# Kernel optimization log

Hardware: AMD Instinct MI355X
Metric: run time of the kernel (lower is better)

Reference implementation:

```python
import jax, jax.numpy as jnp
import numpy as np

N = 50000
E = 800000
N_IN = 256
N_HID = 128
N_OUT = 64
HOP = 10


def setup_inputs() -> dict:
    key = jax.random.key(0)
    ks = jax.random.split(key, 12)
    x = jax.random.normal(ks[0], (N, N_IN), dtype=jnp.float32)
    s = jax.random.randint(ks[1], (E,), 0, N, dtype=jnp.int32)
    t = jax.random.randint(ks[2], (E,), 0, N, dtype=jnp.int32)
    # parameters (xavier-ish scaling)
    fc1W = jax.random.normal(ks[3], (N_HID, N_IN), dtype=jnp.float32) * (1.0 / np.sqrt(N_IN))
    fc1b = jnp.zeros((N_HID,), dtype=jnp.float32)
    fcsW = jax.random.normal(ks[4], (HOP, N_HID, N_HID), dtype=jnp.float32) * (1.0 / np.sqrt(N_HID))
    fcsb = jnp.zeros((HOP, N_HID), dtype=jnp.float32)
    a1 = jax.random.normal(ks[5], (HOP, N_HID), dtype=jnp.float32) * (1.0 / np.sqrt(N_HID))
    a2 = jax.random.normal(ks[6], (HOP, N_HID), dtype=jnp.float32) * (1.0 / np.sqrt(N_HID))
    fc2W = jax.random.normal(ks[7], (N_OUT, N_HID), dtype=jnp.float32) * (1.0 / np.sqrt(N_HID))
    fc2b = jnp.zeros((N_OUT,), dtype=jnp.float32)
    return {"x": x, "s": s, "t": t, "fc1W": fc1W, "fc1b": fc1b,
            "fcsW": fcsW, "fcsb": fcsb, "a1": a1, "a2": a2,
            "fc2W": fc2W, "fc2b": fc2b}


def reference(x, s, t, fc1W, fc1b, fcsW, fcsb, a1, a2, fc2W, fc2b):
    # dropout layers are identity in eval mode
    x = jax.nn.relu(x @ fc1W.T + fc1b)  # [N, n_hid]
    h = x
    for i in range(HOP):
        W, b = fcsW[i], fcsb[i]
        x_new = x @ W.T + b          # [N, n_hid]
        h = h @ W.T + b              # [N, n_hid]
        x1 = x_new @ a1[i]           # [N]
        h1 = h @ a2[i]               # [N]
        w1 = jnp.exp(jax.nn.leaky_relu(x1[s] + h1[t], 0.2))       # [E]
        w2 = jnp.exp(jax.nn.leaky_relu(x1 + x_new @ a2[i], 0.2))  # [N]
        div = jax.ops.segment_sum(w1, s, num_segments=N) + w2     # [N]
        num = jax.ops.segment_sum(w1[:, None] * h[t], s, num_segments=N) + w2[:, None] * x_new
        h = jax.nn.elu(num / div[:, None])
    return h @ fc2W.T + fc2b  # [N, n_out]
```

## Files before the change

### kernel.cpp

```cpp
#include <hip/hip_runtime.h>
#include <math.h>


typedef __attribute__((ext_vector_type(8))) short short8;
typedef __attribute__((ext_vector_type(4))) float f32x4;
#define MFMA16 __builtin_amdgcn_mfma_f32_16x16x32_bf16

__device__ __forceinline__ float lrelu02(float v) { return v > 0.f ? v : 0.2f * v; }

__device__ __forceinline__ float2 bf2f2(unsigned int v) {
    return make_float2(__uint_as_float(v << 16), __uint_as_float(v & 0xffff0000u));
}
__device__ __forceinline__ unsigned int f2bf(float f) {
    unsigned int u = __float_as_uint(f);
    u += 0x7fffu + ((u >> 16) & 1u);
    return u >> 16;
}
__device__ __forceinline__ float hi_part(float f) {
    return __uint_as_float(__float_as_uint(f) & 0xffff0000u);
}
__device__ __forceinline__ uint4 pack_hi(const float4& a, const float4& b) {
    uint4 r;
    r.x = (__float_as_uint(a.x) >> 16) | (__float_as_uint(a.y) & 0xffff0000u);
    r.y = (__float_as_uint(a.z) >> 16) | (__float_as_uint(a.w) & 0xffff0000u);
    r.z = (__float_as_uint(b.x) >> 16) | (__float_as_uint(b.y) & 0xffff0000u);
    r.w = (__float_as_uint(b.z) >> 16) | (__float_as_uint(b.w) & 0xffff0000u);
    return r;
}
__device__ __forceinline__ uint4 pack_lo(const float4& a, const float4& b) {
    uint4 r;
    r.x = f2bf(a.x - hi_part(a.x)) | (f2bf(a.y - hi_part(a.y)) << 16);
    r.y = f2bf(a.z - hi_part(a.z)) | (f2bf(a.w - hi_part(a.w)) << 16);
    r.z = f2bf(b.x - hi_part(b.x)) | (f2bf(b.y - hi_part(b.y)) << 16);
    r.w = f2bf(b.z - hi_part(b.z)) | (f2bf(b.w - hi_part(b.w)) << 16);
    return r;
}

__global__ __launch_bounds__(256) void k_count(const int* __restrict__ s, int* __restrict__ cnt, int E) {
    int e = blockIdx.x * 256 + threadIdx.x;
    if (e < E) atomicAdd(&cnt[s[e]], 1);
}

__global__ __launch_bounds__(256) void k_scan1(const int* __restrict__ cnt, int* __restrict__ bs, int N) {
    __shared__ int sh[256];
    int idx = blockIdx.x * 256 + threadIdx.x;
    sh[threadIdx.x] = (idx < N) ? cnt[idx] : 0;
    __syncthreads();
#pragma unroll
    for (int off = 128; off; off >>= 1) {
        if (threadIdx.x < off) sh[threadIdx.x] += sh[threadIdx.x + off];
        __syncthreads();
    }
    if (threadIdx.x == 0) bs[blockIdx.x] = sh[0];
}

__global__ __launch_bounds__(256) void k_scan2(int* __restrict__ bs, int G) {
    __shared__ int sh[256];
    int t = threadIdx.x;
    int v = (t < G) ? bs[t] : 0;
    sh[t] = v;
    __syncthreads();
    int val = v;
#pragma unroll
    for (int off = 1; off < 256; off <<= 1) {
        int o = (t >= off) ? sh[t - off] : 0;
        __syncthreads();
        val += o; sh[t] = val;
        __syncthreads();
    }
    if (t < G) bs[t] = val - v;
}

__global__ __launch_bounds__(256) void k_scan3(const int* __restrict__ cnt, const int* __restrict__ bs,
                                               int* __restrict__ rp, int N) {
    __shared__ int sh[256];
    int t = threadIdx.x;
    int idx = blockIdx.x * 256 + t;
    int v = (idx < N) ? cnt[idx] : 0;
    sh[t] = v;
    __syncthreads();
    int val = v;
#pragma unroll
    for (int off = 1; off < 256; off <<= 1) {
        int o = (t >= off) ? sh[t - off] : 0;
        __syncthreads();
        val += o; sh[t] = val;
        __syncthreads();
    }
    if (idx <= N) rp[idx] = val - v + bs[blockIdx.x];
}

__global__ __launch_bounds__(256) void k_scatter(const int* __restrict__ s, const int* __restrict__ t,
                                                 const int* __restrict__ rp, int* __restrict__ cursor,
                                                 int* __restrict__ t_sorted, int E) {
    int e = blockIdx.x * 256 + threadIdx.x;
    if (e < E) {
        int u = s[e];
        int pos = atomicAdd(&cursor[u], 1);
        t_sorted[rp[u] + pos] = t[e];
    }
}

__global__ __launch_bounds__(256) void k_wsplit(const float* __restrict__ W,
                                                unsigned short* __restrict__ Whi,
                                                unsigned short* __restrict__ Wlo, int total) {
    int i = blockIdx.x * 256 + threadIdx.x;
    if (i < total) {
        float f = W[i];
        unsigned int u = __float_as_uint(f);
        Whi[i] = (unsigned short)(u >> 16);
        Wlo[i] = (unsigned short)f2bf(f - __uint_as_float(u & 0xffff0000u));
    }
}

__global__ __launch_bounds__(256) void k_prep(
    const float* __restrict__ fcsW, const float* __restrict__ fcsb,
    const float* __restrict__ a1, const float* __restrict__ a2,
    float* __restrict__ Vf, unsigned short* __restrict__ Vh,
    unsigned short* __restrict__ Vl, float* __restrict__ cvec) {
    int i = blockIdx.x;
    int t = threadIdx.x;
    const float* W = fcsW + (size_t)i * 16384;
    if (t < 128) {
        float s1 = 0.f, s2 = 0.f;
        for (int j = 0; j < 128; ++j) {
            float w = W[j * 128 + t];
            s1 = fmaf(w, a1[i * 128 + j], s1);
            s2 = fmaf(w, a2[i * 128 + j], s2);
        }
        Vf[i * 128 + t] = s1;
        Vf[(16 + i) * 128 + t] = s2;
        Vh[i * 128 + t] = (unsigned short)(__float_as_uint(s1) >> 16);
        Vl[i * 128 + t] = (unsigned short)f2bf(s1 - hi_part(s1));
        Vh[(16 + i) * 128 + t] = (unsigned short)(__float_as_uint(s2) >> 16);
        Vl[(16 + i) * 128 + t] = (unsigned short)f2bf(s2 - hi_part(s2));
    } else if (t == 128) {
        float c1 = 0.f, c2 = 0.f;
        for (int j = 0; j < 128; ++j) {
            c1 = fmaf(fcsb[i * 128 + j], a1[i * 128 + j], c1);
            c2 = fmaf(fcsb[i * 128 + j], a2[i * 128 + j], c2);
        }
        cvec[i] = c1;
        cvec[16 + i] = c2;
    }
}

__global__ __launch_bounds__(256) void k_fc1(
    const float* __restrict__ Xf,
    const unsigned short* __restrict__ Wh, const unsigned short* __restrict__ Wl,
    const float* __restrict__ bias,
    unsigned short* __restrict__ Yhi, unsigned short* __restrict__ Ylo, int N) {
    const int tid = threadIdx.x;
    const int r0 = blockIdx.x * 64;
    const int lane = tid & 63;
    const int w = tid >> 6;
    const int wr = (w >> 1) * 32, wc = (w & 1) * 64;
    const int frow = lane & 15;
    const int fk = lane >> 4;
    const int q4 = lane >> 4;

    f32x4 acc[2][4];
#pragma unroll
    for (int i = 0; i < 2; ++i)
#pragma unroll
        for (int j = 0; j < 4; ++j) acc[i][j] = (f32x4){0.f, 0.f, 0.f, 0.f};

    const float4 z4 = make_float4(0.f, 0.f, 0.f, 0.f);
#pragma unroll
    for (int kc = 0; kc < 8; ++kc) {
        short8 ah[2], al[2];
#pragma unroll
        for (int ri = 0; ri < 2; ++ri) {
            int row = r0 + wr + ri * 16 + frow;
            float4 va = z4, vb = z4;
            if (row < N) {
                const float* p = Xf + (size_t)row * 256 + kc * 32 + fk * 8;
                va = *(const float4*)p;
                vb = *(const float4*)(p + 4);
            }
            uint4 h = pack_hi(va, vb);
            uint4 l = pack_lo(va, vb);
            ah[ri] = *(short8*)&h;
            al[ri] = *(short8*)&l;
        }
#pragma unroll
        for (int ci = 0; ci < 4; ++ci) {
            int col = wc + ci * 16 + frow;
            short8 bh = *(const short8*)(Wh + (size_t)col * 256 + kc * 32 + fk * 8);
            short8 bl = *(const short8*)(Wl + (size_t)col * 256 + kc * 32 + fk * 8);
#pragma unroll
            for (int ri = 0; ri < 2; ++ri) {
                acc[ri][ci] = MFMA16(ah[ri], bh, acc[ri][ci], 0, 0, 0);
                acc[ri][ci] = MFMA16(ah[ri], bl, acc[ri][ci], 0, 0, 0);
                acc[ri][ci] = MFMA16(al[ri], bh, acc[ri][ci], 0, 0, 0);
            }
        }
    }

#pragma unroll
    for (int ci = 0; ci < 4; ++ci) {
        int col = wc + ci * 16 + frow;
        float bcol = bias[col];
#pragma unroll
        for (int ri = 0; ri < 2; ++ri) {
            f32x4 v = acc[ri][ci];
#pragma unroll
            for (int reg = 0; reg < 4; ++reg) {
                int grow = r0 + wr + ri * 16 + q4 * 4 + reg;
                if (grow < N) {
                    float val = fmaxf(v[reg] + bcol, 0.f);
                    Yhi[(size_t)grow * 128 + col] = (unsigned short)(__float_as_uint(val) >> 16);
                    Ylo[(size_t)grow * 128 + col] = (unsigned short)f2bf(val - hi_part(val));
                }
            }
        }
    }
}

__global__ __launch_bounds__(256) void k_xdots(
    const unsigned short* __restrict__ Xhi, const unsigned short* __restrict__ Xlo,
    const unsigned short* __restrict__ Vh, const unsigned short* __restrict__ Vl,
    const float* __restrict__ cvec,
    float* __restrict__ x1a_all, float* __restrict__ xa2a_all, int N) {
    const int tid = threadIdx.x;
    const int r0 = blockIdx.x * 64;
    const int lane = tid & 63;
    const int w = tid >> 6;
    const int wr = w * 16;
    const int frow = lane & 15;
    const int fk = lane >> 4;
    const int q4 = lane >> 4;

    f32x4 acc[2];
    acc[0] = (f32x4){0.f, 0.f, 0.f, 0.f};
    acc[1] = (f32x4){0.f, 0.f, 0.f, 0.f};

    const short8 z8 = (short8){0, 0, 0, 0, 0, 0, 0, 0};
#pragma unroll
    for (int kc = 0; kc < 4; ++kc) {
        int row = r0 + wr + frow;
        bool ok = row < N;
        short8 ah = ok ? *(const short8*)(Xhi + (size_t)row * 128 + kc * 32 + fk * 8) : z8;
        short8 al = ok ? *(const short8*)(Xlo + (size_t)row * 128 + kc * 32 + fk * 8) : z8;
#pragma unroll
        for (int ci = 0; ci < 2; ++ci) {
            int col = ci * 16 + frow;
            short8 bh = *(const short8*)(Vh + (size_t)col * 128 + kc * 32 + fk * 8);
            short8 bl = *(const short8*)(Vl + (size_t)col * 128 + kc * 32 + fk * 8);
            acc[ci] = MFMA16(ah, bh, acc[ci], 0, 0, 0);
            acc[ci] = MFMA16(ah, bl, acc[ci], 0, 0, 0);
            acc[ci] = MFMA16(al, bh, acc[ci], 0, 0, 0);
        }
    }

#pragma unroll
    for (int ci = 0; ci < 2; ++ci) {
        int col = ci * 16 + frow;
        float c = cvec[col];
#pragma unroll
        for (int reg = 0; reg < 4; ++reg) {
            int grow = r0 + wr + q4 * 4 + reg;
            if (grow < N) {
                float val = acc[ci][reg] + c;
                if (col < 10) x1a_all[(size_t)col * N + grow] = val;
                else if (col >= 16 && col < 26) xa2a_all[(size_t)(col - 16) * N + grow] = val;
            }
        }
    }
}

__global__ __launch_bounds__(256) void k_gemm(
    const unsigned short* __restrict__ G,
    const unsigned short* __restrict__ Wh, const unsigned short* __restrict__ Wl,
    const float* __restrict__ bias, const float* __restrict__ vnext,
    const float* __restrict__ cnextp,
    unsigned short* __restrict__ Hout, float* __restrict__ h1a, int N) {
    __shared__ unsigned short So[64 * 128];
    __shared__ float dotbuf[64][2];
    const int tid = threadIdx.x;
    const int r0 = blockIdx.x * 64;
    const int lane = tid & 63;
    const int w = tid >> 6;
    const int wr = (w >> 1) * 32, wc = (w & 1) * 64;
    const int frow = lane & 15;
    const int fk = lane >> 4;
    const int q4 = lane >> 4;
    const bool dodot = vnext != nullptr;

    f32x4 acc[2][4];
#pragma unroll
    for (int i = 0; i < 2; ++i)
#pragma unroll
        for (int j = 0; j < 4; ++j) acc[i][j] = (f32x4){0.f, 0.f, 0.f, 0.f};

    const short8 z8 = (short8){0, 0, 0, 0, 0, 0, 0, 0};
#pragma unroll
    for (int kc = 0; kc < 4; ++kc) {
        short8 ah[2];
#pragma unroll
        for (int ri = 0; ri < 2; ++ri) {
            int row = r0 + wr + ri * 16 + frow;
            ah[ri] = (row < N) ? *(const short8*)(G + (size_t)row * 128 + kc * 32 + fk * 8) : z8;
        }
#pragma unroll
        for (int ci = 0; ci < 4; ++ci) {
            int col = wc + ci * 16 + frow;
            short8 bh = *(const short8*)(Wh + (size_t)col * 128 + kc * 32 + fk * 8);
            short8 bl = *(const short8*)(Wl + (size_t)col * 128 + kc * 32 + fk * 8);
#pragma unroll
            for (int ri = 0; ri < 2; ++ri) {
                acc[ri][ci] = MFMA16(ah[ri], bh, acc[ri][ci], 0, 0, 0);
                acc[ri][ci] = MFMA16(ah[ri], bl, acc[ri][ci], 0, 0, 0);
            }
        }
    }

    float dotA[2][4] = {};
#pragma unroll
    for (int ci = 0; ci < 4; ++ci) {
        int col = wc + ci * 16 + frow;
        float bcol = bias[col];
        float vc = dodot ? vnext[col] : 0.f;
#pragma unroll
        for (int ri = 0; ri < 2; ++ri) {
            f32x4 v = acc[ri][ci];
#pragma unroll
            for (int reg = 0; reg < 4; ++reg) {
                float val = v[reg] + bcol;
                val = val > 0.f ? val : expf(val) - 1.f;
                int row = wr + ri * 16 + q4 * 4 + reg;
                int dw = (col >> 1) ^ ((row & 12) << 1);
                So[row * 128 + dw * 2 + (col & 1)] = (unsigned short)f2bf(val);
                dotA[ri][reg] = fmaf(val, vc, dotA[ri][reg]);
            }
        }
    }
#pragma unroll
    for (int m = 1; m < 16; m <<= 1)
#pragma unroll
        for (int ri = 0; ri < 2; ++ri)
#pragma unroll
            for (int reg = 0; reg < 4; ++reg)
                dotA[ri][reg] += __shfl_xor(dotA[ri][reg], m, 64);
    if (frow == 0) {
#pragma unroll
        for (int ri = 0; ri < 2; ++ri)
#pragma unroll
            for (int reg = 0; reg < 4; ++reg) {
                int rl = wr + ri * 16 + q4 * 4 + reg;
                dotbuf[rl][w & 1] = dotA[ri][reg];
            }
    }
    __syncthreads();

#pragma unroll
    for (int q = 0; q < 4; ++q) {
        int idx = q * 256 + tid;
        int row = idx >> 4;
        int gc = idx & 15;
        int dwb = (gc * 4) ^ ((row & 12) << 1);
        uint4 vv = *(const uint4*)(So + row * 128 + dwb * 2);
        int grow = r0 + row;
        if (grow < N) *(uint4*)(Hout + (size_t)grow * 128 + gc * 8) = vv;
    }
    if (dodot && tid < 64) {
        int grow = r0 + tid;
        if (grow < N) h1a[grow] = dotbuf[tid][0] + dotbuf[tid][1] + cnextp[0];
    }
}

__global__ __launch_bounds__(256) void k_agg(
    const unsigned short* __restrict__ xh, const unsigned short* __restrict__ xl,
    const unsigned short* __restrict__ table,
    const float* __restrict__ x1a, const float* __restrict__ xa2a,
    const float* __restrict__ h1a, const int* __restrict__ rp,
    const int* __restrict__ ts,
    unsigned short* __restrict__ g_out, int N) {
    __shared__ uint2 ew[4][64];
    const int wid = threadIdx.x >> 6;
    const int lane = threadIdx.x & 63;
    const int u = blockIdx.x * 4 + wid;
    if (u >= N) return;
    const int l2 = lane << 1;
    float x1u = x1a[u];
    float w2 = expf(lrelu02(x1u + xa2a[u]));
    unsigned int sh = *(const unsigned int*)(xh + (size_t)u * 128 + l2);
    unsigned int sl = *(const unsigned int*)(xl + (size_t)u * 128 + l2);
    float2 hx = bf2f2(sh), lx = bf2f2(sl);
    float accx = w2 * (hx.x + lx.x), accy = w2 * (hx.y + lx.y);
    float div = w2;
    int p0 = rp[u], p1 = rp[u + 1];
    for (int base = p0; base < p1; base += 64) {
        int e = base + lane;
        uint2 pk = make_uint2(0u, 0u);
        if (e < p1) {
            int tv = ts[e];
            pk.x = (unsigned int)tv;
            pk.y = __float_as_uint(expf(lrelu02(x1u + h1a[tv])));
        }
        ew[wid][lane] = pk;
        int m = p1 - base; if (m > 64) m = 64;
        int m8 = (m + 7) & ~7;
        for (int j = 0; j < m8; j += 8) {
            uint2 q[8];
#pragma unroll
            for (int k = 0; k < 8; ++k) q[k] = ew[wid][j + k];
            unsigned int hv[8];
#pragma unroll
            for (int k = 0; k < 8; ++k)
                hv[k] = *(const unsigned int*)(table + (size_t)q[k].x * 128 + l2);
#pragma unroll
            for (int k = 0; k < 8; ++k) {
                float ww = __uint_as_float(q[k].y);
                float2 f = bf2f2(hv[k]);
                accx = fmaf(ww, f.x, accx);
                accy = fmaf(ww, f.y, accy);
                div += ww;
            }
        }
    }
    float ox = accx / div, oy = accy / div;
    *(unsigned int*)(g_out + (size_t)u * 128 + l2) = f2bf(ox) | (f2bf(oy) << 16);
}

__global__ __launch_bounds__(256) void k_fc2(
    const unsigned short* __restrict__ Xhi,
    const unsigned short* __restrict__ Wh, const unsigned short* __restrict__ Wl,
    const float* __restrict__ bias, float* __restrict__ Yf, int N) {
    const int tid = threadIdx.x;
    const int r0 = blockIdx.x * 64;
    const int lane = tid & 63;
    const int w = tid >> 6;
    const int wr = w * 16;
    const int frow = lane & 15;
    const int fk = lane >> 4;
    const int q4 = lane >> 4;

    f32x4 acc[4];
#pragma unroll
    for (int j = 0; j < 4; ++j) acc[j] = (f32x4){0.f, 0.f, 0.f, 0.f};

    const short8 z8 = (short8){0, 0, 0, 0, 0, 0, 0, 0};
#pragma unroll
    for (int kc = 0; kc < 4; ++kc) {
        int row = r0 + wr + frow;
        short8 ah = (row < N) ? *(const short8*)(Xhi + (size_t)row * 128 + kc * 32 + fk * 8) : z8;
#pragma unroll
        for (int ci = 0; ci < 4; ++ci) {
            int col = ci * 16 + frow;
            short8 bh = *(const short8*)(Wh + (size_t)col * 128 + kc * 32 + fk * 8);
            short8 bl = *(const short8*)(Wl + (size_t)col * 128 + kc * 32 + fk * 8);
            acc[ci] = MFMA16(ah, bh, acc[ci], 0, 0, 0);
            acc[ci] = MFMA16(ah, bl, acc[ci], 0, 0, 0);
        }
    }

#pragma unroll
    for (int ci = 0; ci < 4; ++ci) {
        int col = ci * 16 + frow;
        float bcol = bias[col];
#pragma unroll
        for (int reg = 0; reg < 4; ++reg) {
            int grow = r0 + wr + q4 * 4 + reg;
            if (grow < N) Yf[(size_t)grow * 64 + col] = acc[ci][reg] + bcol;
        }
    }
}

extern "C" void kernel_launch(void* const* d_in, const int* in_sizes, int n_in,
                              void* d_out, int out_size, void* d_ws, size_t ws_size,
                              hipStream_t stream) {
    const float* x_in = (const float*)d_in[0];
    const int*   s    = (const int*)d_in[1];
    const int*   t    = (const int*)d_in[2];
    const float* fc1W = (const float*)d_in[3];
    const float* fc1b = (const float*)d_in[4];
    const float* fcsW = (const float*)d_in[5];
    const float* fcsb = (const float*)d_in[6];
    const float* a1   = (const float*)d_in[7];
    const float* a2   = (const float*)d_in[8];
    const float* fc2W = (const float*)d_in[9];
    const float* fc2b = (const float*)d_in[10];

    const int N = in_sizes[0] / 256;
    const int E = in_sizes[1];
    const int G = (N + 255) / 256;
    const int NB64 = (N + 63) / 64;

    char* ws = (char*)d_ws;
    size_t off = 0;
    auto alloc = [&](size_t bytes) -> void* {
        void* p = ws + off;
        off += (bytes + 255) & ~(size_t)255;
        return p;
    };
    unsigned short* xbuf_hi = (unsigned short*)alloc((size_t)N * 128 * 2);
    unsigned short* xbuf_lo = (unsigned short*)alloc((size_t)N * 128 * 2);
    unsigned short* h_hi    = (unsigned short*)alloc((size_t)N * 128 * 2);
    unsigned short* gbuf    = (unsigned short*)alloc((size_t)N * 128 * 2);
    unsigned short* Whi  = (unsigned short*)alloc((size_t)10 * 16384 * 2);
    unsigned short* Wlo  = (unsigned short*)alloc((size_t)10 * 16384 * 2);
    unsigned short* W1hi = (unsigned short*)alloc((size_t)128 * 256 * 2);
    unsigned short* W1lo = (unsigned short*)alloc((size_t)128 * 256 * 2);
    unsigned short* W2hi = (unsigned short*)alloc((size_t)64 * 128 * 2);
    unsigned short* W2lo = (unsigned short*)alloc((size_t)64 * 128 * 2);
    float* Vf   = (float*)alloc((size_t)32 * 128 * 4);
    unsigned short* Vh = (unsigned short*)alloc((size_t)32 * 128 * 2);
    unsigned short* Vl = (unsigned short*)alloc((size_t)32 * 128 * 2);
    float* cvec = (float*)alloc((size_t)32 * 4);
    float* x1a_all  = (float*)alloc((size_t)10 * N * 4);
    float* xa2a_all = (float*)alloc((size_t)10 * N * 4);
    float* h1a  = (float*)alloc((size_t)N * 4);
    int* row_ptr  = (int*)alloc((size_t)(N + 1) * 4);
    int* cnt      = (int*)alloc((size_t)N * 4);
    int* bsums    = (int*)alloc((size_t)1024);
    int* t_sorted = (int*)alloc((size_t)E * 4);

    hipMemsetAsync(cnt, 0, (size_t)N * 4, stream);
    k_count<<<(E + 255) / 256, 256, 0, stream>>>(s, cnt, E);
    k_scan1<<<G, 256, 0, stream>>>(cnt, bsums, N);
    k_scan2<<<1, 256, 0, stream>>>(bsums, G);
    k_scan3<<<G, 256, 0, stream>>>(cnt, bsums, row_ptr, N);
    hipMemsetAsync(cnt, 0, (size_t)N * 4, stream);
    k_scatter<<<(E + 255) / 256, 256, 0, stream>>>(s, t, row_ptr, cnt, t_sorted, E);

    k_wsplit<<<(10 * 16384 + 255) / 256, 256, 0, stream>>>(fcsW, Whi, Wlo, 10 * 16384);
    k_wsplit<<<(128 * 256 + 255) / 256, 256, 0, stream>>>(fc1W, W1hi, W1lo, 128 * 256);
    k_wsplit<<<(64 * 128 + 255) / 256, 256, 0, stream>>>(fc2W, W2hi, W2lo, 64 * 128);
    hipMemsetAsync(Vf, 0, (size_t)32 * 128 * 4, stream);
    hipMemsetAsync(Vh, 0, (size_t)32 * 128 * 2, stream);
    hipMemsetAsync(Vl, 0, (size_t)32 * 128 * 2, stream);
    hipMemsetAsync(cvec, 0, (size_t)32 * 4, stream);
    k_prep<<<10, 256, 0, stream>>>(fcsW, fcsb, a1, a2, Vf, Vh, Vl, cvec);

    k_fc1<<<NB64, 256, 0, stream>>>(x_in, W1hi, W1lo, fc1b, xbuf_hi, xbuf_lo, N);

    k_xdots<<<NB64, 256, 0, stream>>>(xbuf_hi, xbuf_lo, Vh, Vl, cvec,
                                      x1a_all, xa2a_all, N);

    for (int i = 0; i < 10; ++i) {
        const unsigned short* table = (i == 0) ? xbuf_hi : h_hi;
        const float* h1_i = (i == 0) ? (xa2a_all + 0) : h1a;
        k_agg<<<(N + 3) / 4, 256, 0, stream>>>(xbuf_hi, xbuf_lo, table,
                                               x1a_all + (size_t)i * N,
                                               xa2a_all + (size_t)i * N,
                                               h1_i, row_ptr, t_sorted, gbuf, N);
        const float* vnext = (i < 9) ? (Vf + (size_t)(16 + i + 1) * 128) : nullptr;
        const float* cnextp = cvec + (16 + i + 1);
        k_gemm<<<NB64, 256, 0, stream>>>(gbuf, Whi + (size_t)i * 16384,
                                         Wlo + (size_t)i * 16384,
                                         fcsb + (size_t)i * 128, vnext, cnextp,
                                         h_hi, h1a, N);
    }

    k_fc2<<<NB64, 256, 0, stream>>>(h_hi, W2hi, W2lo, fc2b, (float*)d_out, N);
}
```

Baseline: 806.3 us.

## Fuse edge aggregation into per-hop GEMM kernel with ping-pong h buffers

Merges the per-node softmax aggregation kernel and the following 128x128 GEMM into one k_hop kernel. Each 64-row block first aggregates neighbour features into shared memory, then runs MFMA directly from LDS. This removes the gbuf global round-trip and one launch per hop. Because h is now read by other blocks while being written, it ping-pongs between two h buffers and two h1 buffers. The fc1 epilogue is also changed to stage its output through swizzled LDS so it can store 16-byte vectors. Trade-offs: the 64-row grid has far fewer blocks than the old 4-rows-per-block aggregation, so load balance across irregular degrees may suffer. The self term also drops the lo-part of x, which slightly lowers precision.

```diff
diff --git a/kernel.cpp b/kernel.cpp
--- a/kernel.cpp
+++ b/kernel.cpp
@@ -150,6 +150,8 @@
     const unsigned short* __restrict__ Wh, const unsigned short* __restrict__ Wl,
     const float* __restrict__ bias,
     unsigned short* __restrict__ Yhi, unsigned short* __restrict__ Ylo, int N) {
+    __shared__ unsigned short Shi[64 * 128];
+    __shared__ unsigned short Slo[64 * 128];
     const int tid = threadIdx.x;
     const int r0 = blockIdx.x * 64;
     const int lane = tid & 63;
@@ -206,13 +208,25 @@
             f32x4 v = acc[ri][ci];
 #pragma unroll
             for (int reg = 0; reg < 4; ++reg) {
-                int grow = r0 + wr + ri * 16 + q4 * 4 + reg;
-                if (grow < N) {
-                    float val = fmaxf(v[reg] + bcol, 0.f);
-                    Yhi[(size_t)grow * 128 + col] = (unsigned short)(__float_as_uint(val) >> 16);
-                    Ylo[(size_t)grow * 128 + col] = (unsigned short)f2bf(val - hi_part(val));
-                }
-            }
+                float val = fmaxf(v[reg] + bcol, 0.f);
+                int row = wr + ri * 16 + q4 * 4 + reg;
+                int dw = (col >> 1) ^ ((row & 12) << 1);
+                Shi[row * 128 + dw * 2 + (col & 1)] = (unsigned short)(__float_as_uint(val) >> 16);
+                Slo[row * 128 + dw * 2 + (col & 1)] = (unsigned short)f2bf(val - hi_part(val));
+            }
+        }
+    }
+    __syncthreads();
+#pragma unroll
+    for (int q = 0; q < 4; ++q) {
+        int idx = q * 256 + tid;
+        int row = idx >> 4;
+        int gc = idx & 15;
+        int dwb = (gc * 4) ^ ((row & 12) << 1);
+        int grow = r0 + row;
+        if (grow < N) {
+            *(uint4*)(Yhi + (size_t)grow * 128 + gc * 8) = *(const uint4*)(Shi + row * 128 + dwb * 2);
+            *(uint4*)(Ylo + (size_t)grow * 128 + gc * 8) = *(const uint4*)(Slo + row * 128 + dwb * 2);
         }
     }
 }
@@ -269,18 +283,72 @@
     }
 }
 
-__global__ __launch_bounds__(256) void k_gemm(
-    const unsigned short* __restrict__ G,
+__global__ __launch_bounds__(256) void k_hop(
+    const unsigned short* __restrict__ table, const unsigned short* __restrict__ xh,
+    const float* __restrict__ x1a, const float* __restrict__ xa2a,
+    const float* __restrict__ h1in,
+    const int* __restrict__ rp, const int* __restrict__ ts,
     const unsigned short* __restrict__ Wh, const unsigned short* __restrict__ Wl,
     const float* __restrict__ bias, const float* __restrict__ vnext,
     const float* __restrict__ cnextp,
-    unsigned short* __restrict__ Hout, float* __restrict__ h1a, int N) {
-    __shared__ unsigned short So[64 * 128];
+    unsigned short* __restrict__ Hout, float* __restrict__ h1out, int N) {
+    __shared__ unsigned short gS[64 * 128];
+    __shared__ uint2 ew[4][64];
     __shared__ float dotbuf[64][2];
     const int tid = threadIdx.x;
+    const int wid = tid >> 6;
+    const int lane = tid & 63;
     const int r0 = blockIdx.x * 64;
-    const int lane = tid & 63;
-    const int w = tid >> 6;
+
+    for (int j = 0; j < 16; ++j) {
+        int gr = wid * 16 + j;
+        int u = r0 + gr;
+        unsigned int packed = 0u;
+        if (u < N) {
+            float x1u = x1a[u];
+            float w2 = expf(lrelu02(x1u + xa2a[u]));
+            float2 xr = bf2f2(*(const unsigned int*)(xh + (size_t)u * 128 + lane * 2));
+            float accx = w2 * xr.x, accy = w2 * xr.y;
+            float div = w2;
+            int p0 = rp[u], p1 = rp[u + 1];
+            for (int base = p0; base < p1; base += 64) {
+                int e = base + lane;
+                uint2 pk = make_uint2(0u, 0u);
+                if (e < p1) {
+                    int tv = ts[e];
+                    pk.x = (unsigned int)tv;
+                    pk.y = __float_as_uint(expf(lrelu02(x1u + h1in[tv])));
+                }
+                ew[wid][lane] = pk;
+                int m = p1 - base; if (m > 64) m = 64;
+                int m8 = (m + 7) & ~7;
+                for (int jj = 0; jj < m8; jj += 8) {
+                    uint2 q[8];
+#pragma unroll
+                    for (int k = 0; k < 8; ++k) q[k] = ew[wid][jj + k];
+                    unsigned int hv[8];
+#pragma unroll
+                    for (int k = 0; k < 8; ++k)
+                        hv[k] = *(const unsigned int*)(table + (size_t)q[k].x * 128 + lane * 2);
+#pragma unroll
+                    for (int k = 0; k < 8; ++k) {
+                        float ww = __uint_as_float(q[k].y);
+                        float2 f = bf2f2(hv[k]);
+                        accx = fmaf(ww, f.x, accx);
+                        accy = fmaf(ww, f.y, accy);
+                        div += ww;
+                    }
+                }
+            }
+            float ox = accx / div, oy = accy / div;
+            packed = f2bf(ox) | (f2bf(oy) << 16);
+        }
+        int dw = (((lane >> 2) ^ (gr & 7)) << 2) | (lane & 3);
+        *((unsigned int*)gS + gr * 64 + dw) = packed;
+    }
+    __syncthreads();
+
+    const int w = wid;
     const int wr = (w >> 1) * 32, wc = (w & 1) * 64;
     const int frow = lane & 15;
     const int fk = lane >> 4;
@@ -293,14 +361,14 @@
 #pragma unroll
         for (int j = 0; j < 4; ++j) acc[i][j] = (f32x4){0.f, 0.f, 0.f, 0.f};
 
-    const short8 z8 = (short8){0, 0, 0, 0, 0, 0, 0, 0};
 #pragma unroll
     for (int kc = 0; kc < 4; ++kc) {
         short8 ah[2];
 #pragma unroll
         for (int ri = 0; ri < 2; ++ri) {
-            int row = r0 + wr + ri * 16 + frow;
-            ah[ri] = (row < N) ? *(const short8*)(G + (size_t)row * 128 + kc * 32 + fk * 8) : z8;
+            int row = wr + ri * 16 + frow;
+            int gg = kc * 4 + fk;
+            ah[ri] = *(const short8*)(gS + row * 128 + ((gg ^ (row & 7)) * 8));
         }
 #pragma unroll
         for (int ci = 0; ci < 4; ++ci) {
@@ -314,6 +382,7 @@
             }
         }
     }
+    __syncthreads();
 
     float dotA[2][4] = {};
 #pragma unroll
@@ -330,7 +399,7 @@
                 val = val > 0.f ? val : expf(val) - 1.f;
                 int row = wr + ri * 16 + q4 * 4 + reg;
                 int dw = (col >> 1) ^ ((row & 12) << 1);
-                So[row * 128 + dw * 2 + (col & 1)] = (unsigned short)f2bf(val);
+                gS[row * 128 + dw * 2 + (col & 1)] = (unsigned short)f2bf(val);
                 dotA[ri][reg] = fmaf(val, vc, dotA[ri][reg]);
             }
         }
@@ -359,68 +428,14 @@
         int row = idx >> 4;
         int gc = idx & 15;
         int dwb = (gc * 4) ^ ((row & 12) << 1);
-        uint4 vv = *(const uint4*)(So + row * 128 + dwb * 2);
+        uint4 vv = *(const uint4*)(gS + row * 128 + dwb * 2);
         int grow = r0 + row;
         if (grow < N) *(uint4*)(Hout + (size_t)grow * 128 + gc * 8) = vv;
     }
     if (dodot && tid < 64) {
         int grow = r0 + tid;
-        if (grow < N) h1a[grow] = dotbuf[tid][0] + dotbuf[tid][1] + cnextp[0];
-    }
-}
-
-__global__ __launch_bounds__(256) void k_agg(
-    const unsigned short* __restrict__ xh, const unsigned short* __restrict__ xl,
-    const unsigned short* __restrict__ table,
-    const float* __restrict__ x1a, const float* __restrict__ xa2a,
-    const float* __restrict__ h1a, const int* __restrict__ rp,
-    const int* __restrict__ ts,
-    unsigned short* __restrict__ g_out, int N) {
-    __shared__ uint2 ew[4][64];
-    const int wid = threadIdx.x >> 6;
-    const int lane = threadIdx.x & 63;
-    const int u = blockIdx.x * 4 + wid;
-    if (u >= N) return;
-    const int l2 = lane << 1;
-    float x1u = x1a[u];
-    float w2 = expf(lrelu02(x1u + xa2a[u]));
-    unsigned int sh = *(const unsigned int*)(xh + (size_t)u * 128 + l2);
-    unsigned int sl = *(const unsigned int*)(xl + (size_t)u * 128 + l2);
-    float2 hx = bf2f2(sh), lx = bf2f2(sl);
-    float accx = w2 * (hx.x + lx.x), accy = w2 * (hx.y + lx.y);
-    float div = w2;
-    int p0 = rp[u], p1 = rp[u + 1];
-    for (int base = p0; base < p1; base += 64) {
-        int e = base + lane;
-        uint2 pk = make_uint2(0u, 0u);
-        if (e < p1) {
-            int tv = ts[e];
-            pk.x = (unsigned int)tv;
-            pk.y = __float_as_uint(expf(lrelu02(x1u + h1a[tv])));
-        }
-        ew[wid][lane] = pk;
-        int m = p1 - base; if (m > 64) m = 64;
-        int m8 = (m + 7) & ~7;
-        for (int j = 0; j < m8; j += 8) {
-            uint2 q[8];
-#pragma unroll
-            for (int k = 0; k < 8; ++k) q[k] = ew[wid][j + k];
-            unsigned int hv[8];
-#pragma unroll
-            for (int k = 0; k < 8; ++k)
-                hv[k] = *(const unsigned int*)(table + (size_t)q[k].x * 128 + l2);
-#pragma unroll
-            for (int k = 0; k < 8; ++k) {
-                float ww = __uint_as_float(q[k].y);
-                float2 f = bf2f2(hv[k]);
-                accx = fmaf(ww, f.x, accx);
-                accy = fmaf(ww, f.y, accy);
-                div += ww;
-            }
-        }
-    }
-    float ox = accx / div, oy = accy / div;
-    *(unsigned int*)(g_out + (size_t)u * 128 + l2) = f2bf(ox) | (f2bf(oy) << 16);
+        if (grow < N) h1out[grow] = dotbuf[tid][0] + dotbuf[tid][1] + cnextp[0];
+    }
 }
 
 __global__ __launch_bounds__(256) void k_fc2(
@@ -496,8 +511,8 @@
     };
     unsigned short* xbuf_hi = (unsigned short*)alloc((size_t)N * 128 * 2);
     unsigned short* xbuf_lo = (unsigned short*)alloc((size_t)N * 128 * 2);
-    unsigned short* h_hi    = (unsigned short*)alloc((size_t)N * 128 * 2);
-    unsigned short* gbuf    = (unsigned short*)alloc((size_t)N * 128 * 2);
+    unsigned short* hA      = (unsigned short*)alloc((size_t)N * 128 * 2);
+    unsigned short* hB      = (unsigned short*)alloc((size_t)N * 128 * 2);
     unsigned short* Whi  = (unsigned short*)alloc((size_t)10 * 16384 * 2);
     unsigned short* Wlo  = (unsigned short*)alloc((size_t)10 * 16384 * 2);
     unsigned short* W1hi = (unsigned short*)alloc((size_t)128 * 256 * 2);
@@ -510,7 +525,8 @@
     float* cvec = (float*)alloc((size_t)32 * 4);
     float* x1a_all  = (float*)alloc((size_t)10 * N * 4);
     float* xa2a_all = (float*)alloc((size_t)10 * N * 4);
-    float* h1a  = (float*)alloc((size_t)N * 4);
+    float* h1aA = (float*)alloc((size_t)N * 4);
+    float* h1aB = (float*)alloc((size_t)N * 4);
     int* row_ptr  = (int*)alloc((size_t)(N + 1) * 4);
     int* cnt      = (int*)alloc((size_t)N * 4);
     int* bsums    = (int*)alloc((size_t)1024);
@@ -538,20 +554,21 @@
     k_xdots<<<NB64, 256, 0, stream>>>(xbuf_hi, xbuf_lo, Vh, Vl, cvec,
                                       x1a_all, xa2a_all, N);
 
+    const unsigned short* table = xbuf_hi;
+    const float* h1in = xa2a_all;
     for (int i = 0; i < 10; ++i) {
-        const unsigned short* table = (i == 0) ? xbuf_hi : h_hi;
-        const float* h1_i = (i == 0) ? (xa2a_all + 0) : h1a;
-        k_agg<<<(N + 3) / 4, 256, 0, stream>>>(xbuf_hi, xbuf_lo, table,
-                                               x1a_all + (size_t)i * N,
-                                               xa2a_all + (size_t)i * N,
-                                               h1_i, row_ptr, t_sorted, gbuf, N);
+        unsigned short* hout = (i & 1) ? hB : hA;
+        float* h1out = (i & 1) ? h1aB : h1aA;
         const float* vnext = (i < 9) ? (Vf + (size_t)(16 + i + 1) * 128) : nullptr;
-        const float* cnextp = cvec + (16 + i + 1);
-        k_gemm<<<NB64, 256, 0, stream>>>(gbuf, Whi + (size_t)i * 16384,
-                                         Wlo + (size_t)i * 16384,
-                                         fcsb + (size_t)i * 128, vnext, cnextp,
-                                         h_hi, h1a, N);
-    }
-
-    k_fc2<<<NB64, 256, 0, stream>>>(h_hi, W2hi, W2lo, fc2b, (float*)d_out, N);
-}
+        k_hop<<<NB64, 256, 0, stream>>>(table, xbuf_hi,
+                                        x1a_all + (size_t)i * N, xa2a_all + (size_t)i * N,
+                                        h1in, row_ptr, t_sorted,
+                                        Whi + (size_t)i * 16384, Wlo + (size_t)i * 16384,
+                                        fcsb + (size_t)i * 128, vnext, cvec + (16 + i + 1),
+                                        hout, h1out, N);
+        table = hout;
+        h1in = h1out;
+    }
+
+    k_fc2<<<NB64, 256, 0, stream>>>(table, W2hi, W2lo, fc2b, (float*)d_out, N);
+}
```

Measured after the change: 789.7 us. 1.02x faster.

## Split neighbor aggregation into column slices and stage fc1 output through LDS

Applied to the files above, without the earlier changes.

Replaces the per-node aggregation kernel with a gather kernel where each wave handles one node's 32-column slice: four 16-lane groups each process a different edge, and edge weights and targets are broadcast via shuffles instead of LDS. Interleaving four slice blocks per row group is meant to improve L2 locality and parallelism for the random gathers. The self term now uses only the high bf16 part of x, a small precision loss. fc1's epilogue also writes through swizzled shared memory to get coalesced 16-byte global stores.

```diff
diff --git a/kernel.cpp b/kernel.cpp
--- a/kernel.cpp
+++ b/kernel.cpp
@@ -150,6 +150,8 @@
     const unsigned short* __restrict__ Wh, const unsigned short* __restrict__ Wl,
     const float* __restrict__ bias,
     unsigned short* __restrict__ Yhi, unsigned short* __restrict__ Ylo, int N) {
+    __shared__ unsigned short Shi[64 * 128];
+    __shared__ unsigned short Slo[64 * 128];
     const int tid = threadIdx.x;
     const int r0 = blockIdx.x * 64;
     const int lane = tid & 63;
@@ -206,13 +208,25 @@
             f32x4 v = acc[ri][ci];
 #pragma unroll
             for (int reg = 0; reg < 4; ++reg) {
-                int grow = r0 + wr + ri * 16 + q4 * 4 + reg;
-                if (grow < N) {
-                    float val = fmaxf(v[reg] + bcol, 0.f);
-                    Yhi[(size_t)grow * 128 + col] = (unsigned short)(__float_as_uint(val) >> 16);
-                    Ylo[(size_t)grow * 128 + col] = (unsigned short)f2bf(val - hi_part(val));
-                }
-            }
+                float val = fmaxf(v[reg] + bcol, 0.f);
+                int row = wr + ri * 16 + q4 * 4 + reg;
+                int dw = (col >> 1) ^ ((row & 12) << 1);
+                Shi[row * 128 + dw * 2 + (col & 1)] = (unsigned short)(__float_as_uint(val) >> 16);
+                Slo[row * 128 + dw * 2 + (col & 1)] = (unsigned short)f2bf(val - hi_part(val));
+            }
+        }
+    }
+    __syncthreads();
+#pragma unroll
+    for (int q = 0; q < 4; ++q) {
+        int idx = q * 256 + tid;
+        int row = idx >> 4;
+        int gc = idx & 15;
+        int dwb = (gc * 4) ^ ((row & 12) << 1);
+        int grow = r0 + row;
+        if (grow < N) {
+            *(uint4*)(Yhi + (size_t)grow * 128 + gc * 8) = *(const uint4*)(Shi + row * 128 + dwb * 2);
+            *(uint4*)(Ylo + (size_t)grow * 128 + gc * 8) = *(const uint4*)(Slo + row * 128 + dwb * 2);
         }
     }
 }
@@ -267,6 +281,62 @@
             }
         }
     }
+}
+
+__global__ __launch_bounds__(256) void k_gather(
+    const unsigned short* __restrict__ table, const unsigned short* __restrict__ xh,
+    const float* __restrict__ x1a, const float* __restrict__ xa2a,
+    const float* __restrict__ h1in,
+    const int* __restrict__ rp, const int* __restrict__ ts,
+    unsigned short* __restrict__ gout, int N, int RG) {
+    const int r = (int)blockIdx.x & 7;
+    const int qb = (int)blockIdx.x >> 3;
+    const int slice = r >> 1;
+    const int rg = qb * 2 + (r & 1);
+    if (rg >= RG) return;
+    const int wid = threadIdx.x >> 6;
+    const int lane = threadIdx.x & 63;
+    const int u = rg * 4 + wid;
+    if (u >= N) return;
+    const int m = lane & 15;
+    const int qw = lane >> 4;
+
+    float x1u = x1a[u];
+    float w2 = expf(lrelu02(x1u + xa2a[u]));
+    float accx = 0.f, accy = 0.f, divp = 0.f;
+    int p0 = rp[u], p1 = rp[u + 1];
+    for (int base = p0; base < p1; base += 64) {
+        int e = base + lane;
+        int tv = 0;
+        float wv = 0.f;
+        if (e < p1) {
+            tv = ts[e];
+            wv = expf(lrelu02(x1u + h1in[tv]));
+        }
+        divp += wv;
+        int mm = p1 - base; if (mm > 64) mm = 64;
+        for (int j = 0; j < mm; j += 4) {
+            int jj = j + qw;
+            float w = __shfl(wv, jj & 63, 64);
+            int tt = __shfl(tv, jj & 63, 64);
+            if (jj >= mm) w = 0.f;
+            unsigned int hv = *(const unsigned int*)(table + (size_t)tt * 128 + slice * 32 + m * 2);
+            float2 f = bf2f2(hv);
+            accx = fmaf(w, f.x, accx);
+            accy = fmaf(w, f.y, accy);
+        }
+    }
+#pragma unroll
+    for (int o = 1; o < 64; o <<= 1) divp += __shfl_xor(divp, o, 64);
+    accx += __shfl_xor(accx, 16, 64); accx += __shfl_xor(accx, 32, 64);
+    accy += __shfl_xor(accy, 16, 64); accy += __shfl_xor(accy, 32, 64);
+    float rdiv = 1.f / (divp + w2);
+    unsigned int xv = *(const unsigned int*)(xh + (size_t)u * 128 + slice * 32 + m * 2);
+    float2 xf = bf2f2(xv);
+    float gx = rdiv * (accx + w2 * xf.x);
+    float gy = rdiv * (accy + w2 * xf.y);
+    if (qw == 0)
+        *(unsigned int*)(gout + (size_t)u * 128 + slice * 32 + m * 2) = f2bf(gx) | (f2bf(gy) << 16);
 }
 
 __global__ __launch_bounds__(256) void k_gemm(
@@ -336,12 +406,12 @@
         }
     }
 #pragma unroll
-    for (int m = 1; m < 16; m <<= 1)
+    for (int mm = 1; mm < 16; mm <<= 1)
 #pragma unroll
         for (int ri = 0; ri < 2; ++ri)
 #pragma unroll
             for (int reg = 0; reg < 4; ++reg)
-                dotA[ri][reg] += __shfl_xor(dotA[ri][reg], m, 64);
+                dotA[ri][reg] += __shfl_xor(dotA[ri][reg], mm, 64);
     if (frow == 0) {
 #pragma unroll
         for (int ri = 0; ri < 2; ++ri)
@@ -367,60 +437,6 @@
         int grow = r0 + tid;
         if (grow < N) h1a[grow] = dotbuf[tid][0] + dotbuf[tid][1] + cnextp[0];
     }
-}
-
-__global__ __launch_bounds__(256) void k_agg(
-    const unsigned short* __restrict__ xh, const unsigned short* __restrict__ xl,
-    const unsigned short* __restrict__ table,
-    const float* __restrict__ x1a, const float* __restrict__ xa2a,
-    const float* __restrict__ h1a, const int* __restrict__ rp,
-    const int* __restrict__ ts,
-    unsigned short* __restrict__ g_out, int N) {
-    __shared__ uint2 ew[4][64];
-    const int wid = threadIdx.x >> 6;
-    const int lane = threadIdx.x & 63;
-    const int u = blockIdx.x * 4 + wid;
-    if (u >= N) return;
-    const int l2 = lane << 1;
-    float x1u = x1a[u];
-    float w2 = expf(lrelu02(x1u + xa2a[u]));
-    unsigned int sh = *(const unsigned int*)(xh + (size_t)u * 128 + l2);
-    unsigned int sl = *(const unsigned int*)(xl + (size_t)u * 128 + l2);
-    float2 hx = bf2f2(sh), lx = bf2f2(sl);
-    float accx = w2 * (hx.x + lx.x), accy = w2 * (hx.y + lx.y);
-    float div = w2;
-    int p0 = rp[u], p1 = rp[u + 1];
-    for (int base = p0; base < p1; base += 64) {
-        int e = base + lane;
-        uint2 pk = make_uint2(0u, 0u);
-        if (e < p1) {
-            int tv = ts[e];
-            pk.x = (unsigned int)tv;
-            pk.y = __float_as_uint(expf(lrelu02(x1u + h1a[tv])));
-        }
-        ew[wid][lane] = pk;
-        int m = p1 - base; if (m > 64) m = 64;
-        int m8 = (m + 7) & ~7;
-        for (int j = 0; j < m8; j += 8) {
-            uint2 q[8];
-#pragma unroll
-            for (int k = 0; k < 8; ++k) q[k] = ew[wid][j + k];
-            unsigned int hv[8];
-#pragma unroll
-            for (int k = 0; k < 8; ++k)
-                hv[k] = *(const unsigned int*)(table + (size_t)q[k].x * 128 + l2);
-#pragma unroll
-            for (int k = 0; k < 8; ++k) {
-                float ww = __uint_as_float(q[k].y);
-                float2 f = bf2f2(hv[k]);
-                accx = fmaf(ww, f.x, accx);
-                accy = fmaf(ww, f.y, accy);
-                div += ww;
-            }
-        }
-    }
-    float ox = accx / div, oy = accy / div;
-    *(unsigned int*)(g_out + (size_t)u * 128 + l2) = f2bf(ox) | (f2bf(oy) << 16);
 }
 
 __global__ __launch_bounds__(256) void k_fc2(
@@ -486,6 +502,8 @@
     const int E = in_sizes[1];
     const int G = (N + 255) / 256;
     const int NB64 = (N + 63) / 64;
+    const int RG = (N + 3) / 4;
+    const int GGRID = 8 * ((RG + 1) / 2);
 
     char* ws = (char*)d_ws;
     size_t off = 0;
@@ -496,7 +514,7 @@
     };
     unsigned short* xbuf_hi = (unsigned short*)alloc((size_t)N * 128 * 2);
     unsigned short* xbuf_lo = (unsigned short*)alloc((size_t)N * 128 * 2);
-    unsigned short* h_hi    = (unsigned short*)alloc((size_t)N * 128 * 2);
+    unsigned short* hbuf    = (unsigned short*)alloc((size_t)N * 128 * 2);
     unsigned short* gbuf    = (unsigned short*)alloc((size_t)N * 128 * 2);
     unsigned short* Whi  = (unsigned short*)alloc((size_t)10 * 16384 * 2);
     unsigned short* Wlo  = (unsigned short*)alloc((size_t)10 * 16384 * 2);
@@ -538,20 +556,20 @@
     k_xdots<<<NB64, 256, 0, stream>>>(xbuf_hi, xbuf_lo, Vh, Vl, cvec,
                                       x1a_all, xa2a_all, N);
 
+    const unsigned short* table = xbuf_hi;
+    const float* h1in = xa2a_all;
     for (int i = 0; i < 10; ++i) {
-        const unsigned short* table = (i == 0) ? xbuf_hi : h_hi;
-        const float* h1_i = (i == 0) ? (xa2a_all + 0) : h1a;
-        k_agg<<<(N + 3) / 4, 256, 0, stream>>>(xbuf_hi, xbuf_lo, table,
-                                               x1a_all + (size_t)i * N,
-                                               xa2a_all + (size_t)i * N,
-                                               h1_i, row_ptr, t_sorted, gbuf, N);
+        k_gather<<<GGRID, 256, 0, stream>>>(table, xbuf_hi,
+                                            x1a_all + (size_t)i * N, xa2a_all + (size_t)i * N,
+                                            h1in, row_ptr, t_sorted, gbuf, N, RG);
         const float* vnext = (i < 9) ? (Vf + (size_t)(16 + i + 1) * 128) : nullptr;
-        const float* cnextp = cvec + (16 + i + 1);
         k_gemm<<<NB64, 256, 0, stream>>>(gbuf, Whi + (size_t)i * 16384,
                                          Wlo + (size_t)i * 16384,
-                                         fcsb + (size_t)i * 128, vnext, cnextp,
-                                         h_hi, h1a, N);
-    }
-
-    k_fc2<<<NB64, 256, 0, stream>>>(h_hi, W2hi, W2lo, fc2b, (float*)d_out, N);
-}
+                                         fcsb + (size_t)i * 128, vnext, cvec + (16 + i + 1),
+                                         hbuf, h1a, N);
+        table = hbuf;
+        h1in = h1a;
+    }
+
+    k_fc2<<<NB64, 256, 0, stream>>>(table, W2hi, W2lo, fc2b, (float*)d_out, N);
+}
```

Result: slower. 1.438 ms (+78.4%).
